# Kernel tuning notes

Measured on AMD Instinct MI355X. Metric: run time of the kernel, lower is better.

The kernel has to match this reference:

```python
import jax, jax.numpy as jnp
import numpy as np

B, D, H, W, C = 2, 8, 56, 56, 384
NH = 12
HD = C // NH
WIN = (2, 7, 7)
SHIFT = (1, 3, 3)
TDIM = 384
RANK = C // 8
HID = 4 * C
N = WIN[0] * WIN[1] * WIN[2]  # 98 tokens per window
NW = (D // WIN[0]) * (H // WIN[1]) * (W // WIN[2])  # windows per batch element


def _rel_index():
    wd, wh, ww = WIN
    coords = np.stack(np.meshgrid(np.arange(wd), np.arange(wh), np.arange(ww), indexing='ij'))
    coords = coords.reshape(3, -1)  # (3, N)
    rel = (coords[:, :, None] - coords[:, None, :]).transpose(1, 2, 0)  # (N, N, 3)
    rel[..., 0] += wd - 1; rel[..., 1] += wh - 1; rel[..., 2] += ww - 1
    rel[..., 0] *= (2 * wh - 1) * (2 * ww - 1)
    rel[..., 1] *= (2 * ww - 1)
    return rel.sum(-1)  # (N, N) int

REL_IDX = _rel_index()


def _wpart_np(x):
    b, d, h, w, c = x.shape
    x = x.reshape(b, d // WIN[0], WIN[0], h // WIN[1], WIN[1], w // WIN[2], WIN[2], c)
    return x.transpose(0, 1, 3, 5, 2, 4, 6, 7).reshape(-1, N, c)


def _attn_mask():
    # faithful port of compute_mask (note: only 2 slices along W, as in source)
    wd, wh, ww = WIN
    sd, sh, sw = SHIFT
    img = np.zeros((1, D, H, W, 1), np.float32)
    cnt = 0
    for ds in (slice(-wd), slice(-wd, -sd), slice(-sd, None)):
        for hs in (slice(-wh), slice(-wh, -sh), slice(-sh, None)):
            for ws in (slice(-ww), slice(-ww, None)):
                img[:, ds, hs, ws, :] = cnt
                cnt += 1
    mw = _wpart_np(img).squeeze(-1)  # (nW, N)
    am = mw[:, None, :] - mw[:, :, None]  # (nW, N, N)
    return np.where(am != 0, np.float32(-100.0), np.float32(0.0))

ATTN_MASK = _attn_mask()


def wpart(x):
    b, c = x.shape[0], x.shape[-1]
    x = x.reshape(b, D // WIN[0], WIN[0], H // WIN[1], WIN[1], W // WIN[2], WIN[2], c)
    return x.transpose(0, 1, 3, 5, 2, 4, 6, 7).reshape(-1, N, c)


def wrev(win):
    c = win.shape[-1]
    x = win.reshape(B, D // WIN[0], H // WIN[1], W // WIN[2], WIN[0], WIN[1], WIN[2], c)
    return x.transpose(0, 1, 4, 2, 5, 3, 6, 7).reshape(B, D, H, W, c)


def ln(x):
    m = x.mean(-1, keepdims=True)
    v = ((x - m) ** 2).mean(-1, keepdims=True)
    return (x - m) / jnp.sqrt(v + 1e-6)


def window_attn(xw, qkv_w, qkv_b, proj_w, proj_b, rel_bias, mask):
    Bw = xw.shape[0]
    qkv = (xw @ qkv_w + qkv_b).reshape(Bw, N, 3, NH, HD).transpose(2, 0, 3, 1, 4)
    q, k, v = qkv[0] * (HD ** -0.5), qkv[1], qkv[2]
    a = jnp.einsum('bhnd,bhmd->bhnm', q, k)  # (Bw, NH, N, N)
    bias = rel_bias[REL_IDX.reshape(-1)].reshape(N, N, NH).transpose(2, 0, 1)
    a = a + bias[None]
    a = a.reshape(Bw // NW, NW, NH, N, N) + mask[None, :, None]
    a = jax.nn.softmax(a.reshape(Bw, NH, N, N), axis=-1)
    out = jnp.einsum('bhnm,bhmd->bhnd', a, v).transpose(0, 2, 1, 3).reshape(Bw, N, C)
    return out @ proj_w + proj_b


def setup_inputs() -> dict:
    key = jax.random.key(0)
    ks = jax.random.split(key, 16)
    s = 0.02
    return {
        'x': jax.random.normal(ks[0], (B, D, H, W, C), jnp.float32),
        't': jax.random.normal(ks[1], (B, TDIM), jnp.float32),
        'qkv_w': jax.random.normal(ks[2], (C, 3 * C), jnp.float32) * s,
        'qkv_b': jax.random.normal(ks[3], (3 * C,), jnp.float32) * s,
        'proj_w': jax.random.normal(ks[4], (C, C), jnp.float32) * s,
        'proj_b': jax.random.normal(ks[5], (C,), jnp.float32) * s,
        'rel_bias': jax.random.normal(ks[6], ((2 * WIN[0] - 1) * (2 * WIN[1] - 1) * (2 * WIN[2] - 1), NH), jnp.float32) * s,
        'fc1_w': jax.random.normal(ks[7], (C, HID), jnp.float32) * s,
        'fc1_b': jax.random.normal(ks[8], (HID,), jnp.float32) * s,
        'fc2_w': jax.random.normal(ks[9], (HID, C), jnp.float32) * s,
        'fc2_b': jax.random.normal(ks[10], (C,), jnp.float32) * s,
        'ada_w1': jax.random.normal(ks[11], (TDIM, RANK), jnp.float32) * s,
        'ada_w2': jax.random.normal(ks[12], (RANK, 6 * C), jnp.float32) * s,
        'ada_b2': jax.random.normal(ks[13], (6 * C,), jnp.float32) * s,
    }


def reference(x, t, qkv_w, qkv_b, proj_w, proj_b, rel_bias, fc1_w, fc1_b, fc2_w, fc2_b, ada_w1, ada_w2, ada_b2):
    mask = jnp.asarray(ATTN_MASK)
    mod = jax.nn.silu(t) @ ada_w1 @ ada_w2 + ada_b2  # (B, 6C)
    s_msa, sc_msa, g_msa, s_mlp, sc_mlp, g_mlp = jnp.split(mod, 6, axis=1)

    def mod5(h, sh, sc):
        return h * (1 + sc[:, None, None, None, :]) + sh[:, None, None, None, :]

    # attention branch (shifted-window MSA)
    h = mod5(ln(x), s_msa, sc_msa)
    hs = jnp.roll(h, shift=(-SHIFT[0], -SHIFT[1], -SHIFT[2]), axis=(1, 2, 3))
    aw = window_attn(wpart(hs), qkv_w, qkv_b, proj_w, proj_b, rel_bias, mask)
    hs = wrev(aw)
    h = jnp.roll(hs, shift=SHIFT, axis=(1, 2, 3))
    x = x + g_msa[:, None, None, None, :] * h

    # MLP branch
    h2 = mod5(ln(x), s_mlp, sc_mlp)
    m = jax.nn.gelu(h2 @ fc1_w + fc1_b, approximate=False) @ fc2_w + fc2_b
    return x + g_mlp[:, None, None, None, :] * m
```

## Files before the change

kernel.cpp:

```cpp
#include <hip/hip_runtime.h>
#include <hip/hip_bf16.h>
#include <math.h>

using bf16 = __hip_bfloat16;
typedef __bf16 bf16x8 __attribute__((ext_vector_type(8)));
typedef float f32x4 __attribute__((ext_vector_type(4)));
typedef unsigned int u32;


__device__ __forceinline__ void async_cp16(const void* g, void* l) {
  __builtin_amdgcn_global_load_lds(
      (const __attribute__((address_space(1))) u32*)g,
      (__attribute__((address_space(3))) u32*)l, 16, 0, 0);
}

__device__ __forceinline__ int row_to_gidx(int row) {
  int win = row / 98, tok = row - win * 98;
  int b = win >> 8, wd = (win >> 6) & 3, wh = (win >> 3) & 7, ww = win & 7;
  int td = tok / 49, rem = tok - td * 49;
  int th = rem / 7, tw = rem - th * 7;
  int od = (wd * 2 + td + 1) & 7;
  int oh = wh * 7 + th + 3; if (oh >= 56) oh -= 56;
  int ow = ww * 7 + tw + 3; if (ow >= 56) ow -= 56;
  return ((b * 8 + od) * 56 + oh) * 56 + ow;
}

__global__ __launch_bounds__(256) void mod_kernel(
    const float* __restrict__ t, const float* __restrict__ w1,
    const float* __restrict__ w2, const float* __restrict__ b2,
    float* __restrict__ modout)
{
  __shared__ float u[2 * 48];
  int tid = threadIdx.x;
  if (tid < 96) {
    int b = tid / 48, r = tid - (tid / 48) * 48;
    float acc = 0.f;
    for (int k = 0; k < 384; ++k) {
      float x = t[b * 384 + k];
      float s = x / (1.f + __expf(-x));
      acc += s * w1[k * 48 + r];
    }
    u[b * 48 + r] = acc;
  }
  __syncthreads();
  for (int idx = tid; idx < 2 * 2304; idx += 256) {
    int b = idx / 2304, c = idx - b * 2304;
    float acc = b2[c];
    #pragma unroll
    for (int k = 0; k < 48; ++k) acc += u[b * 48 + k] * w2[k * 2304 + c];
    modout[idx] = acc;
  }
}

__global__ __launch_bounds__(256) void wconv_kernel(
    const float* __restrict__ W, bf16* __restrict__ Wt, int K, int N)
{
  int idx = blockIdx.x * 256 + threadIdx.x;
  if (idx < K * N) {
    int k = idx / N, n = idx - k * N;
    Wt[(size_t)n * K + k] = __float2bfloat16(W[idx]);
  }
}

__global__ __launch_bounds__(256) void bm_kernel(
    const float* __restrict__ relb, bf16* __restrict__ bm)
{
  int idx = blockIdx.x * 256 + threadIdx.x;
  if (idx >= 4 * 12 * 112 * 112) return;
  int j = idx % 112, tmp = idx / 112;
  int i = tmp % 112; tmp /= 112;
  int h = tmp % 12, p = tmp / 12;
  float v;
  if (i < 98 && j < 98) {
    int tdi = i / 49, ri = i % 49, thi = ri / 7, twi = ri % 7;
    int tdj = j / 49, rj = j % 49, thj = rj / 7, twj = rj % 7;
    int ridx = (tdi - tdj + 1) * 169 + (thi - thj + 6) * 13 + (twi - twj + 6);
    bool msk = ((p & 2) && (tdi != tdj)) || ((p & 1) && ((thi < 4) != (thj < 4)));
    v = relb[ridx * 12 + h] + (msk ? -100.f : 0.f);
  } else {
    v = -1e38f;
  }
  bm[idx] = __float2bfloat16(v);
}

template <int PHASE>
__global__ __launch_bounds__(256) void ln_mod_kernel(
    const float* __restrict__ src, const float* __restrict__ modv,
    bf16* __restrict__ dst)
{
  int wid = threadIdx.x >> 6, lane = threadIdx.x & 63;
  int row = blockIdx.x * 4 + wid;
  int gtok;
  if (PHASE == 0) gtok = row_to_gidx(row); else gtok = row;
  int b = row / 25088;
  const float* s = src + (size_t)gtok * 384;
  float vals[6], sum = 0.f, sq = 0.f;
  #pragma unroll
  for (int i = 0; i < 6; ++i) {
    float v = s[lane + i * 64];
    vals[i] = v; sum += v; sq += v * v;
  }
  #pragma unroll
  for (int o = 32; o; o >>= 1) { sum += __shfl_xor(sum, o, 64); sq += __shfl_xor(sq, o, 64); }
  float mean = sum * (1.f / 384.f);
  float var = sq * (1.f / 384.f) - mean * mean;
  float rstd = rsqrtf(var + 1e-6f);
  int mb = b * 2304 + (PHASE == 0 ? 0 : 1152);
  #pragma unroll
  for (int i = 0; i < 6; ++i) {
    int c = lane + i * 64;
    float scv = modv[mb + 384 + c], shv = modv[mb + c];
    dst[(size_t)row * 384 + c] = __float2bfloat16((vals[i] - mean) * rstd * (1.f + scv) + shv);
  }
}

template <int EPI>
__global__ __launch_bounds__(256) void gemm128_kernel(
    const bf16* __restrict__ A, const bf16* __restrict__ Bt,
    const float* __restrict__ bias, const int N, const int K,
    bf16* __restrict__ outB, float* __restrict__ outF,
    const float* __restrict__ resid, const float* __restrict__ modv)
{
  __shared__ bf16 sA[128 * 32];
  __shared__ bf16 sB[128 * 32];
  const int tid = threadIdx.x;
  const int lane = tid & 63, wid = tid >> 6;
  const int wm = wid >> 1, wn = wid & 1;
  const int row0 = blockIdx.y * 128, col0 = blockIdx.x * 128;

  const int lrow = lane & 15, lk8 = (lane >> 4) << 3;
  const int r0 = tid >> 2, c0 = (tid & 3) << 3;

  const f32x4 vzero = {0.f, 0.f, 0.f, 0.f};
  f32x4 acc[4][4];
  #pragma unroll
  for (int m = 0; m < 4; ++m)
    #pragma unroll
    for (int n = 0; n < 4; ++n) acc[m][n] = vzero;

  const bf16* Arow0 = A + (size_t)(row0 + r0) * K + c0;
  const bf16* Arow1 = A + (size_t)(row0 + r0 + 64) * K + c0;
  const bf16* Brow0 = Bt + (size_t)(col0 + r0) * K + c0;
  const bf16* Brow1 = Bt + (size_t)(col0 + r0 + 64) * K + c0;

  for (int kt = 0; kt < K; kt += 32) {
    __syncthreads();
    async_cp16(Arow0 + kt, sA + (size_t)tid * 8);
    async_cp16(Arow1 + kt, sA + (size_t)(tid + 256) * 8);
    async_cp16(Brow0 + kt, sB + (size_t)tid * 8);
    async_cp16(Brow1 + kt, sB + (size_t)(tid + 256) * 8);
    asm volatile("s_waitcnt vmcnt(0)" ::: "memory");
    __syncthreads();
    bf16x8 af[4], bfv[4];
    #pragma unroll
    for (int m = 0; m < 4; ++m)
      af[m] = *(const bf16x8*)(sA + (wm * 64 + m * 16 + lrow) * 32 + lk8);
    #pragma unroll
    for (int n = 0; n < 4; ++n)
      bfv[n] = *(const bf16x8*)(sB + (wn * 64 + n * 16 + lrow) * 32 + lk8);
    #pragma unroll
    for (int m = 0; m < 4; ++m)
      #pragma unroll
      for (int n = 0; n < 4; ++n)
        acc[m][n] = __builtin_amdgcn_mfma_f32_16x16x32_bf16(af[m], bfv[n], acc[m][n], 0, 0, 0);
  }

  #pragma unroll
  for (int m = 0; m < 4; ++m) {
    #pragma unroll
    for (int r = 0; r < 4; ++r) {
      const int row = row0 + wm * 64 + m * 16 + (lane >> 4) * 4 + r;
      int gofs = 0, b = 0;
      if (EPI == 1) { gofs = row_to_gidx(row) * 384; b = row / 25088; }
      if (EPI == 3) { gofs = row * 384; b = row / 25088; }
      #pragma unroll
      for (int n = 0; n < 4; ++n) {
        const int col = col0 + wn * 64 + n * 16 + (lane & 15);
        float v = acc[m][n][r] + bias[col];
        if (EPI == 0) {
          outB[(size_t)row * N + col] = __float2bfloat16(v);
        } else if (EPI == 2) {
          float g = 0.5f * v * (1.f + erff(v * 0.70710678118654752f));
          outB[(size_t)row * N + col] = __float2bfloat16(g);
        } else if (EPI == 1) {
          outF[gofs + col] = resid[gofs + col] + modv[b * 2304 + 768 + col] * v;
        } else {
          outF[gofs + col] = resid[gofs + col] + modv[b * 2304 + 1920 + col] * v;
        }
      }
    }
  }
}

__global__ __launch_bounds__(256) void attn_kernel(
    const bf16* __restrict__ qkv, const bf16* __restrict__ bm,
    bf16* __restrict__ outp)
{
  __shared__ bf16 k_s[112][40];
  __shared__ bf16 v_t[32][136];
  __shared__ bf16 p_s[4][16][136];

  const int head = blockIdx.x;
  const int win = blockIdx.y;
  const int tid = threadIdx.x;
  const int lane = tid & 63, wid = tid >> 6;
  const int g = lane >> 4, c16 = lane & 15;
  const size_t rowbase = (size_t)win * 98;
  const bf16 zero = __float2bfloat16(0.f);

  for (int lin = tid; lin < 448; lin += 256) {
    int row = lin >> 2, ch = (lin & 3) << 3;
    uint4 val = make_uint4(0, 0, 0, 0);
    if (row < 98)
      val = *(const uint4*)(qkv + (rowbase + row) * 1152 + 384 + head * 32 + ch);
    *(uint4*)&k_s[row][ch] = val;
  }
  for (int lin = tid; lin < 4096; lin += 256) {
    int d = lin & 31, tok = lin >> 5;
    bf16 val = zero;
    if (tok < 98) val = qkv[(rowbase + tok) * 1152 + 768 + head * 32 + d];
    v_t[d][tok] = val;
  }
  for (int lin = tid; lin < 1536; lin += 256) {
    int w = lin / 384, rem = lin - w * 384;
    p_s[w][rem / 24][112 + rem % 24] = zero;
  }
  __syncthreads();

  const int p = ((((win >> 6) & 3) == 3) ? 2 : 0) | ((((win >> 3) & 7) == 7) ? 1 : 0);
  const bf16* bmrow = bm + (size_t)(p * 12 + head) * 12544;
  const float scale = 0.17677669529663687f;
  const f32x4 vzero = {0.f, 0.f, 0.f, 0.f};

  for (int s = wid; s < 7; s += 4) {
    const int q0 = s * 16;
    int qrow = q0 + c16; if (qrow > 97) qrow = 97;
    bf16x8 qf = *(const bf16x8*)(qkv + (rowbase + qrow) * 1152 + head * 32 + g * 8);

    f32x4 sa[7];
    #pragma unroll
    for (int ct = 0; ct < 7; ++ct) {
      bf16x8 kf = *(const bf16x8*)&k_s[ct * 16 + c16][g * 8];
      sa[ct] = __builtin_amdgcn_mfma_f32_16x16x32_bf16(qf, kf, vzero, 0, 0, 0);
    }

    float sv[7][4];
    float mrow[4] = {-1e30f, -1e30f, -1e30f, -1e30f};
    #pragma unroll
    for (int ct = 0; ct < 7; ++ct) {
      #pragma unroll
      for (int r = 0; r < 4; ++r) {
        int i = q0 + g * 4 + r, j = ct * 16 + c16;
        float val = sa[ct][r] * scale + __bfloat162float(bmrow[i * 112 + j]);
        sv[ct][r] = val;
        mrow[r] = fmaxf(mrow[r], val);
      }
    }
    #pragma unroll
    for (int r = 0; r < 4; ++r) {
      #pragma unroll
      for (int off = 1; off < 16; off <<= 1)
        mrow[r] = fmaxf(mrow[r], __shfl_xor(mrow[r], off, 64));
    }
    float rsum[4] = {0.f, 0.f, 0.f, 0.f};
    #pragma unroll
    for (int ct = 0; ct < 7; ++ct) {
      #pragma unroll
      for (int r = 0; r < 4; ++r) {
        float e = __expf(sv[ct][r] - mrow[r]);
        sv[ct][r] = e;
        rsum[r] += e;
      }
    }
    #pragma unroll
    for (int r = 0; r < 4; ++r) {
      #pragma unroll
      for (int off = 1; off < 16; off <<= 1)
        rsum[r] += __shfl_xor(rsum[r], off, 64);
      rsum[r] = 1.f / rsum[r];
    }
    #pragma unroll
    for (int ct = 0; ct < 7; ++ct)
      #pragma unroll
      for (int r = 0; r < 4; ++r)
        p_s[wid][g * 4 + r][ct * 16 + c16] = __float2bfloat16(sv[ct][r] * rsum[r]);

    asm volatile("s_waitcnt lgkmcnt(0)" ::: "memory");

    f32x4 o0 = vzero, o1 = vzero;
    #pragma unroll
    for (int kk = 0; kk < 4; ++kk) {
      bf16x8 pa = *(const bf16x8*)&p_s[wid][c16][kk * 32 + g * 8];
      bf16x8 v0 = *(const bf16x8*)&v_t[c16][kk * 32 + g * 8];
      bf16x8 v1 = *(const bf16x8*)&v_t[16 + c16][kk * 32 + g * 8];
      o0 = __builtin_amdgcn_mfma_f32_16x16x32_bf16(pa, v0, o0, 0, 0, 0);
      o1 = __builtin_amdgcn_mfma_f32_16x16x32_bf16(pa, v1, o1, 0, 0, 0);
    }
    #pragma unroll
    for (int r = 0; r < 4; ++r) {
      int qi = q0 + g * 4 + r;
      if (qi < 98) {
        size_t ob = (rowbase + qi) * 384 + head * 32;
        outp[ob + c16] = __float2bfloat16(o0[r]);
        outp[ob + 16 + c16] = __float2bfloat16(o1[r]);
      }
    }
  }
}

extern "C" void kernel_launch(void* const* d_in, const int* in_sizes, int n_in,
                              void* d_out, int out_size, void* d_ws, size_t ws_size,
                              hipStream_t stream)
{
  (void)in_sizes; (void)n_in; (void)out_size; (void)ws_size;
  const float* x      = (const float*)d_in[0];
  const float* t      = (const float*)d_in[1];
  const float* qkv_w  = (const float*)d_in[2];
  const float* qkv_b  = (const float*)d_in[3];
  const float* proj_w = (const float*)d_in[4];
  const float* proj_b = (const float*)d_in[5];
  const float* relb   = (const float*)d_in[6];
  const float* fc1_w  = (const float*)d_in[7];
  const float* fc1_b  = (const float*)d_in[8];
  const float* fc2_w  = (const float*)d_in[9];
  const float* fc2_b  = (const float*)d_in[10];
  const float* ada_w1 = (const float*)d_in[11];
  const float* ada_w2 = (const float*)d_in[12];
  const float* ada_b2 = (const float*)d_in[13];
  float* out = (float*)d_out;
  char* ws = (char*)d_ws;

  float* modbuf = (float*)(ws + 0);
  bf16* wqkv_t  = (bf16*)(ws + 18432);
  bf16* wproj_t = (bf16*)(ws + 903168);
  bf16* wfc1_t  = (bf16*)(ws + 1198080);
  bf16* wfc2_t  = (bf16*)(ws + 2377728);
  bf16* bufA    = (bf16*)(ws + 3557376);
  bf16* qkvbuf  = (bf16*)(ws + 42092544);
  bf16* bufB    = (bf16*)(ws + 42092544 + 115605504);
  bf16* midbuf  = (bf16*)(ws + 42092544);
  bf16* bmbuf   = bufA;

  wconv_kernel<<<(384 * 1152 + 255) / 256, 256, 0, stream>>>(qkv_w, wqkv_t, 384, 1152);
  wconv_kernel<<<(384 * 384 + 255) / 256, 256, 0, stream>>>(proj_w, wproj_t, 384, 384);
  wconv_kernel<<<(384 * 1536 + 255) / 256, 256, 0, stream>>>(fc1_w, wfc1_t, 384, 1536);
  wconv_kernel<<<(1536 * 384 + 255) / 256, 256, 0, stream>>>(fc2_w, wfc2_t, 1536, 384);

  mod_kernel<<<1, 256, 0, stream>>>(t, ada_w1, ada_w2, ada_b2, modbuf);

  ln_mod_kernel<0><<<12544, 256, 0, stream>>>(x, modbuf, bufA);

  gemm128_kernel<0><<<dim3(9, 392), 256, 0, stream>>>(bufA, wqkv_t, qkv_b, 1152, 384,
                                                      qkvbuf, nullptr, nullptr, nullptr);

  bm_kernel<<<2352, 256, 0, stream>>>(relb, bmbuf);

  attn_kernel<<<dim3(12, 512), 256, 0, stream>>>(qkvbuf, bmbuf, bufB);

  gemm128_kernel<1><<<dim3(3, 392), 256, 0, stream>>>(bufB, wproj_t, proj_b, 384, 384,
                                                      nullptr, out, x, modbuf);

  ln_mod_kernel<1><<<12544, 256, 0, stream>>>(out, modbuf, bufA);

  gemm128_kernel<2><<<dim3(12, 392), 256, 0, stream>>>(bufA, wfc1_t, fc1_b, 1536, 384,
                                                       midbuf, nullptr, nullptr, nullptr);

  gemm128_kernel<3><<<dim3(3, 392), 256, 0, stream>>>(midbuf, wfc2_t, fc2_b, 384, 1536,
                                                      nullptr, out, out, modbuf);
}
```

Baseline: 613.4 us.

## Double-buffer GEMM LDS tiles, swizzle LDS layout, remap workgroups across XCDs

After: 566.2 us. 7.7% less time.

```diff
diff --git a/kernel.cpp b/kernel.cpp
--- a/kernel.cpp
+++ b/kernel.cpp
@@ -121,15 +121,24 @@
     bf16* __restrict__ outB, float* __restrict__ outF,
     const float* __restrict__ resid, const float* __restrict__ modv)
 {
-  __shared__ bf16 sA[128 * 32];
-  __shared__ bf16 sB[128 * 32];
+  __shared__ bf16 sA[2][128 * 32];
+  __shared__ bf16 sB[2][128 * 32];
   const int tid = threadIdx.x;
   const int lane = tid & 63, wid = tid >> 6;
   const int wm = wid >> 1, wn = wid & 1;
-  const int row0 = blockIdx.y * 128, col0 = blockIdx.x * 128;
-
-  const int lrow = lane & 15, lk8 = (lane >> 4) << 3;
-  const int r0 = tid >> 2, c0 = (tid & 3) << 3;
+
+  const int gx = gridDim.x;
+  const int nwg = gx * (int)gridDim.y;
+  const int orig = (int)blockIdx.y * gx + (int)blockIdx.x;
+  const int q = nwg >> 3;
+  const int wg = (orig & 7) * q + (orig >> 3);
+  const int bx = wg % gx, by = wg / gx;
+  const int row0 = by * 128, col0 = bx * 128;
+
+  const int lrow = lane & 15;
+  const int sl8 = (((lane >> 4) ^ ((lane >> 1) & 3)) << 3);
+  const int r0 = tid >> 2;
+  const int c0 = (((tid & 3) ^ ((tid >> 3) & 3)) << 3);
 
   const f32x4 vzero = {0.f, 0.f, 0.f, 0.f};
   f32x4 acc[4][4];
@@ -143,27 +152,39 @@
   const bf16* Brow0 = Bt + (size_t)(col0 + r0) * K + c0;
   const bf16* Brow1 = Bt + (size_t)(col0 + r0 + 64) * K + c0;
 
-  for (int kt = 0; kt < K; kt += 32) {
-    __syncthreads();
-    async_cp16(Arow0 + kt, sA + (size_t)tid * 8);
-    async_cp16(Arow1 + kt, sA + (size_t)(tid + 256) * 8);
-    async_cp16(Brow0 + kt, sB + (size_t)tid * 8);
-    async_cp16(Brow1 + kt, sB + (size_t)(tid + 256) * 8);
+  auto stage = [&](int b, int kt) {
+    async_cp16(Arow0 + kt, &sA[b][(size_t)tid * 8]);
+    async_cp16(Arow1 + kt, &sA[b][(size_t)(tid + 256) * 8]);
+    async_cp16(Brow0 + kt, &sB[b][(size_t)tid * 8]);
+    async_cp16(Brow1 + kt, &sB[b][(size_t)(tid + 256) * 8]);
+  };
+  auto compute = [&](int cb) {
+    bf16x8 af[4], bfv[4];
+    #pragma unroll
+    for (int m = 0; m < 4; ++m)
+      af[m] = *(const bf16x8*)(&sA[cb][(wm * 64 + m * 16 + lrow) * 32 + sl8]);
+    #pragma unroll
+    for (int n = 0; n < 4; ++n)
+      bfv[n] = *(const bf16x8*)(&sB[cb][(wn * 64 + n * 16 + lrow) * 32 + sl8]);
+    #pragma unroll
+    for (int m = 0; m < 4; ++m)
+      #pragma unroll
+      for (int n = 0; n < 4; ++n)
+        acc[m][n] = __builtin_amdgcn_mfma_f32_16x16x32_bf16(af[m], bfv[n], acc[m][n], 0, 0, 0);
+  };
+
+  stage(0, 0);
+  asm volatile("s_waitcnt vmcnt(0)" ::: "memory");
+  __syncthreads();
+  int cur = 0;
+  for (int kt = 32; kt < K; kt += 32) {
+    stage(cur ^ 1, kt);
+    compute(cur);
     asm volatile("s_waitcnt vmcnt(0)" ::: "memory");
     __syncthreads();
-    bf16x8 af[4], bfv[4];
-    #pragma unroll
-    for (int m = 0; m < 4; ++m)
-      af[m] = *(const bf16x8*)(sA + (wm * 64 + m * 16 + lrow) * 32 + lk8);
-    #pragma unroll
-    for (int n = 0; n < 4; ++n)
-      bfv[n] = *(const bf16x8*)(sB + (wn * 64 + n * 16 + lrow) * 32 + lk8);
-    #pragma unroll
-    for (int m = 0; m < 4; ++m)
-      #pragma unroll
-      for (int n = 0; n < 4; ++n)
-        acc[m][n] = __builtin_amdgcn_mfma_f32_16x16x32_bf16(af[m], bfv[n], acc[m][n], 0, 0, 0);
-  }
+    cur ^= 1;
+  }
+  compute(cur);
 
   #pragma unroll
   for (int m = 0; m < 4; ++m) {
```
